# Kernel optimization log

Measured on AMD Instinct MI355X. Metric: run time of the kernel, lower is better.

Reference implementation:

```python
import jax, jax.numpy as jnp
import numpy as np

S_GRID = 7
B_BOX = 2
N_CLS = 20
N_CH = B_BOX * 5 + N_CLS  # 30
LAMBDA_OBJ = 5.0
LAMBDA_NOOBJ = 0.5
CI = np.array([4, 9])
BI = np.array([0, 1, 2, 3, 5, 6, 7, 8])


def setup_inputs() -> dict:
    key = jax.random.key(0)
    k1, k2 = jax.random.split(key)
    batch = 512
    P = jax.random.uniform(k1, (batch, S_GRID, S_GRID, N_CH), dtype=jnp.float32)
    T = jax.random.uniform(k2, (batch, S_GRID, S_GRID, N_CH), dtype=jnp.float32)
    # deterministic object mask: 1/8 of cells are 'object' cells (channel 4 == 1 exactly)
    cell_idx = jnp.arange(batch * S_GRID * S_GRID).reshape(batch, S_GRID, S_GRID)
    obj_mask = (cell_idx % 8 == 0).astype(jnp.float32)
    T = T.at[..., 4].set(obj_mask)
    return {"P": P, "T": T}


def _norm2dnorm(b, S):
    # (cx, cy, w, h) -> (x1, y1, x2, y2) with cx,cy divided by S
    xy = b[:, :2] / S
    wh = b[:, 2:]
    return jnp.concatenate([xy - 0.5 * wh, xy + 0.5 * wh], axis=-1)


def _iou_mat(b1, b2):
    # b1: (N,4), b2: (M,4) -> (N,M) IoU
    lt = jnp.maximum(b1[:, None, :2], b2[None, :, :2])
    rb = jnp.minimum(b1[:, None, 2:], b2[None, :, 2:])
    wh = jnp.clip(rb - lt, 0.0)
    inter = wh[..., 0] * wh[..., 1]
    a1 = (b1[:, 2] - b1[:, 0]) * (b1[:, 3] - b1[:, 1])
    a2 = (b2[:, 2] - b2[:, 0]) * (b2[:, 3] - b2[:, 1])
    return inter / (a1[:, None] + a2[None, :] - inter)


def reference(P, T):
    batch = P.shape[0]
    Pf = P.reshape(-1, N_CH)
    Tf = T.reshape(-1, N_CH)
    # masks computed on concrete data (static counts by construction)
    obj = np.asarray(Tf[:, 4] == 1.0)
    coord_idx = jnp.asarray(np.nonzero(obj)[0])
    noobj_idx = jnp.asarray(np.nonzero(~obj)[0])

    coordP = Pf[coord_idx]
    coordT = Tf[coord_idx]
    noobjP = Pf[noobj_idx]
    noobjT = Tf[noobj_idx]

    ClassP = coordP[:, B_BOX * 5:]
    ClassT = coordT[:, B_BOX * 5:]
    NoObjP = noobjP[:, CI].reshape(-1)
    NoObjT = noobjT[:, CI].reshape(-1)
    ConfP = coordP[:, CI].reshape(-1)          # (2*Ncoord,)
    BBoxP = coordP[:, BI].reshape(-1, 4)       # (2*Ncoord, 4)
    BBoxT = coordT[:, BI].reshape(-1, 4)

    # original torch code does this under no_grad -> stop_gradient
    BP = jax.lax.stop_gradient(_norm2dnorm(BBoxP, float(S_GRID)))
    BT = jax.lax.stop_gradient(_norm2dnorm(BBoxT, float(S_GRID)))
    M = _iou_mat(BP, BT)                       # (NSize, NSize)
    iou = jax.lax.stop_gradient(jnp.max(M, axis=0))
    idx = jnp.argmax(M, axis=0)                # best pred row per target column

    BPg = BP[idx]
    BTg = BT[idx]
    ConfPg = ConfP[idx]

    lossXY = jnp.sum((BPg[:, :2] - BTg[:, :2]) ** 2)
    lossWH = jnp.sum((jnp.sqrt(BPg[:, 2:]) - jnp.sqrt(BTg[:, 2:])) ** 2)
    lossObj = jnp.sum((ConfPg - iou) ** 2)
    lossNObj = jnp.sum((NoObjP - NoObjT) ** 2)
    lossClass = jnp.sum((ClassP - ClassT) ** 2)

    return (LAMBDA_OBJ * (lossXY + lossWH) + LAMBDA_NOOBJ * lossNObj + (lossObj + lossClass)) / batch
```

## Files before the change

kernel.cpp:

```cpp
#include <hip/hip_runtime.h>
#include <stdint.h>

#define S_GRID 7
#define N_CH 30
#define MAXB 8192
#define NTILE 32
#define NCHUNK 80

typedef float float8 __attribute__((ext_vector_type(8)));


__global__ void k_init(float* __restrict__ acc, int* __restrict__ ctr, int* __restrict__ finalCtr) {
    if (threadIdx.x < 4)  acc[threadIdx.x] = 0.0f;
    if (threadIdx.x == 4) *ctr = 0;
    if (threadIdx.x == 5) *finalCtr = 0;
}

__global__ void k_prep(const float* __restrict__ P, const float* __restrict__ T, int ncell,
                       int* __restrict__ ctr,
                       float8* __restrict__ PB8, float4* __restrict__ BT4,
                       float* __restrict__ acc,
                       unsigned long long* __restrict__ maxkey) {
    int gid = blockIdx.x * 256 + threadIdx.x;
    if (gid < MAXB) maxkey[gid] = 0ull;

    int cell = gid;
    float2 pr[15], tr[15];
    if (cell < ncell) {
        const float2* p2 = (const float2*)(P + (size_t)cell * N_CH);
        const float2* t2 = (const float2*)(T + (size_t)cell * N_CH);
        #pragma unroll
        for (int k = 0; k < 15; ++k) { pr[k] = p2[k]; tr[k] = t2[k]; }
    } else {
        #pragma unroll
        for (int k = 0; k < 15; ++k) { pr[k] = make_float2(0.f, 0.f); tr[k] = make_float2(0.f, 0.f); }
    }
    bool obj = (cell < ncell) && (tr[2].x == 1.0f);

    int lane = threadIdx.x & 63;
    unsigned long long bm = __ballot(obj);
    int wcnt = __popcll(bm);
    int base = 0;
    if (lane == 0 && wcnt) base = atomicAdd(ctr, wcnt);
    base = __shfl(base, 0);

    float cls = 0.f, nob = 0.f;
    if (cell < ncell) {
        if (obj) {
            #pragma unroll
            for (int k = 5; k < 15; ++k) {
                float d0 = pr[k].x - tr[k].x, d1 = pr[k].y - tr[k].y;
                cls += d0 * d0 + d1 * d1;
            }
        } else {
            float d0 = pr[2].x - tr[2].x;
            float d1 = pr[4].y - tr[4].y;
            nob = d0 * d0 + d1 * d1;
        }
    }
    #pragma unroll
    for (int o = 32; o; o >>= 1) { cls += __shfl_down(cls, o); nob += __shfl_down(nob, o); }
    if (lane == 0) {
        if (cls != 0.f) atomicAdd(&acc[3], cls);
        if (nob != 0.f) atomicAdd(&acc[2], nob);
    }

    if (obj) {
        int rank = base + __popcll(bm & ((1ull << lane) - 1ull));
        float bx[2][5] = {
            { pr[0].x, pr[0].y, pr[1].x, pr[1].y, pr[2].x },
            { pr[2].y, pr[3].x, pr[3].y, pr[4].x, pr[4].y }
        };
        float tx[2][4] = {
            { tr[0].x, tr[0].y, tr[1].x, tr[1].y },
            { tr[2].y, tr[3].x, tr[3].y, tr[4].x }
        };
        #pragma unroll
        for (int bb = 0; bb < 2; ++bb) {
            int m = 2 * rank + bb;
            if (m < MAXB) {
                float cx = bx[bb][0] / (float)S_GRID, cy = bx[bb][1] / (float)S_GRID;
                float w = bx[bb][2], h = bx[bb][3];
                float8 v;
                v[0] = cx - 0.5f * w; v[1] = cy - 0.5f * h;
                v[2] = cx + 0.5f * w; v[3] = cy + 0.5f * h;
                v[4] = (v[2] - v[0]) * (v[3] - v[1]);
                v[5] = bx[bb][4];
                v[6] = 0.f; v[7] = 0.f;
                PB8[m] = v;
                cx = tx[bb][0] / (float)S_GRID; cy = tx[bb][1] / (float)S_GRID;
                w = tx[bb][2]; h = tx[bb][3];
                BT4[m] = make_float4(cx - 0.5f * w, cy - 0.5f * h, cx + 0.5f * w, cy + 0.5f * h);
            }
        }
    }
}

__global__ void k_match(const float8* __restrict__ PB8, const float4* __restrict__ BT4,
                        const int* __restrict__ ctr,
                        unsigned long long* __restrict__ maxkey) {
    int nb = 2 * (*ctr); if (nb > MAXB) nb = MAXB;
    int tid = threadIdx.x;
    int j = blockIdx.x * 256 + tid;
    if (blockIdx.x * 256 >= nb) return;
    int c = blockIdx.y;
    int chunkLen = (((nb + NCHUNK - 1) / NCHUNK) + 3) & ~3;
    int i0 = c * chunkLen;
    int i1 = min(nb, i0 + chunkLen);
    if (i0 >= i1) return;

    float4 tb = BT4[min(j, nb - 1)];
    float ta = (tb.z - tb.x) * (tb.w - tb.y);
    float bI = -1.f, bS = 1.f;
    int bidx = 0;

    float8 n0 = PB8[i0], n1 = PB8[i0 + 1], n2 = PB8[i0 + 2], n3 = PB8[i0 + 3];
    for (int ib = i0; ib < i1; ib += 4) {
        float8 c0 = n0, c1 = n1, c2 = n2, c3 = n3;
        int nx = ib + 4;
        if (nx < i1) { n0 = PB8[nx]; n1 = PB8[nx + 1]; n2 = PB8[nx + 2]; n3 = PB8[nx + 3]; }
        #define STEP(cc, kk)  {                                                     \
            float lx = fmaxf(tb.x, cc[0]), ly = fmaxf(tb.y, cc[1]);                 \
            float rx = fminf(tb.z, cc[2]), ry = fminf(tb.w, cc[3]);                 \
            float wx = fmaxf(rx - lx, 0.f), wy = fmaxf(ry - ly, 0.f);               \
            float inter = wx * wy;                                                  \
            float sum = ta + cc[4];                                                 \
            bool win = (inter * bS > bI * sum) && ((ib + kk) < i1);                 \
            bI   = win ? inter      : bI;                                           \
            bS   = win ? sum        : bS;                                           \
            bidx = win ? (ib + kk)  : bidx;                                         \
        }
        STEP(c0, 0) STEP(c1, 1) STEP(c2, 2) STEP(c3, 3)
        #undef STEP
    }

    if (j < nb && bI >= 0.f) {
        float iou = bI / (bS - bI);
        unsigned long long key =
            ((unsigned long long)__float_as_uint(iou) << 32) |
            (unsigned long long)(0xFFFFFFFFu - (unsigned)bidx);
        atomicMax(&maxkey[j], key);
    }
}

__global__ void k_final(const float8* __restrict__ PB8, const float4* __restrict__ BT4,
                        const int* __restrict__ ctr,
                        const unsigned long long* __restrict__ maxkey,
                        float* __restrict__ acc, int* __restrict__ finalCtr,
                        float* __restrict__ out, float inv_batch) {
    int nb = 2 * (*ctr); if (nb > MAXB) nb = MAXB;
    int tid = threadIdx.x;
    int j = blockIdx.x * 256 + tid;
    float sxywh = 0.f, sobj = 0.f;
    if (j < nb) {
        unsigned long long key = maxkey[j];
        float iou = __uint_as_float((unsigned)(key >> 32));
        unsigned idx = 0xFFFFFFFFu - (unsigned)(key & 0xFFFFFFFFull);
        float8 pb = PB8[idx];
        float4 bt = BT4[idx];
        float dx = pb[0] - bt.x, dy = pb[1] - bt.y;
        float dw = sqrtf(pb[2]) - sqrtf(bt.z);
        float dh = sqrtf(pb[3]) - sqrtf(bt.w);
        sxywh = dx * dx + dy * dy + dw * dw + dh * dh;
        float dob = pb[5] - iou;
        sobj = dob * dob;
    }
    #pragma unroll
    for (int o = 32; o; o >>= 1) { sxywh += __shfl_down(sxywh, o); sobj += __shfl_down(sobj, o); }
    if ((tid & 63) == 0) {
        if (sxywh != 0.f) atomicAdd(&acc[0], sxywh);
        if (sobj != 0.f)  atomicAdd(&acc[1], sobj);
    }
    __syncthreads();
    if (tid == 0) {
        int old = __hip_atomic_fetch_add(finalCtr, 1, __ATOMIC_ACQ_REL, __HIP_MEMORY_SCOPE_AGENT);
        if (old == NTILE - 1) {
            float a0 = __hip_atomic_load(&acc[0], __ATOMIC_RELAXED, __HIP_MEMORY_SCOPE_AGENT);
            float a1 = __hip_atomic_load(&acc[1], __ATOMIC_RELAXED, __HIP_MEMORY_SCOPE_AGENT);
            float a2 = __hip_atomic_load(&acc[2], __ATOMIC_RELAXED, __HIP_MEMORY_SCOPE_AGENT);
            float a3 = __hip_atomic_load(&acc[3], __ATOMIC_RELAXED, __HIP_MEMORY_SCOPE_AGENT);
            out[0] = (5.0f * a0 + 0.5f * a2 + a1 + a3) * inv_batch;
        }
    }
}

extern "C" void kernel_launch(void* const* d_in, const int* in_sizes, int n_in,
                              void* d_out, int out_size, void* d_ws, size_t ws_size,
                              hipStream_t stream) {
    const float* P = (const float*)d_in[0];
    const float* T = (const float*)d_in[1];
    int ncell = in_sizes[0] / N_CH;
    int batch = ncell / (S_GRID * S_GRID);

    char* ws = (char*)d_ws;
    float* acc      = (float*)ws;
    int*   ctr      = (int*)(ws + 16);
    int*   finalCtr = (int*)(ws + 20);
    unsigned long long* maxkey = (unsigned long long*)(ws + 1024);
    float8* PB8 = (float8*)(ws + 66560);
    float4* BT4 = (float4*)(ws + 328704);

    int nblk = (ncell + 255) / 256;
    k_init <<<1, 64, 0, stream>>>(acc, ctr, finalCtr);
    k_prep <<<nblk, 256, 0, stream>>>(P, T, ncell, ctr, PB8, BT4, acc, maxkey);
    dim3 g3(NTILE, NCHUNK);
    k_match<<<g3, 256, 0, stream>>>(PB8, BT4, ctr, maxkey);
    k_final<<<NTILE, 256, 0, stream>>>(PB8, BT4, ctr, maxkey, acc, finalCtr,
                                       (float*)d_out, 1.0f / (float)batch);
}
```

Baseline: 59.17 us.

## Stage predicted boxes in LDS as float4 and recompute area in match kernel

Predicted boxes are now stored as a compact float4 array, with confidence moved to a separate ConfP array, instead of a padded float8 that carried a precomputed area. Each k_match block copies its chunk of prediction boxes into shared memory once, and every thread then reads from LDS rather than issuing its own global or L1 loads. The box area is recomputed per pair, which adds a few FLOPs in the inner loop, and a __syncthreads is added per block. The goal is to halve the bytes per box and cut redundant global-load traffic in the O(N^2) IoU matching loop.

```diff
diff --git a/kernel.cpp b/kernel.cpp
--- a/kernel.cpp
+++ b/kernel.cpp
@@ -6,8 +6,7 @@
 #define MAXB 8192
 #define NTILE 32
 #define NCHUNK 80
-
-typedef float float8 __attribute__((ext_vector_type(8)));
+#define CHUNK_MAX 104
 
 
 __global__ void k_init(float* __restrict__ acc, int* __restrict__ ctr, int* __restrict__ finalCtr) {
@@ -18,7 +17,8 @@
 
 __global__ void k_prep(const float* __restrict__ P, const float* __restrict__ T, int ncell,
                        int* __restrict__ ctr,
-                       float8* __restrict__ PB8, float4* __restrict__ BT4,
+                       float4* __restrict__ PB4, float4* __restrict__ BT4,
+                       float* __restrict__ ConfP,
                        float* __restrict__ acc,
                        unsigned long long* __restrict__ maxkey) {
     int gid = blockIdx.x * 256 + threadIdx.x;
@@ -81,13 +81,8 @@
             if (m < MAXB) {
                 float cx = bx[bb][0] / (float)S_GRID, cy = bx[bb][1] / (float)S_GRID;
                 float w = bx[bb][2], h = bx[bb][3];
-                float8 v;
-                v[0] = cx - 0.5f * w; v[1] = cy - 0.5f * h;
-                v[2] = cx + 0.5f * w; v[3] = cy + 0.5f * h;
-                v[4] = (v[2] - v[0]) * (v[3] - v[1]);
-                v[5] = bx[bb][4];
-                v[6] = 0.f; v[7] = 0.f;
-                PB8[m] = v;
+                PB4[m] = make_float4(cx - 0.5f * w, cy - 0.5f * h, cx + 0.5f * w, cy + 0.5f * h);
+                ConfP[m] = bx[bb][4];
                 cx = tx[bb][0] / (float)S_GRID; cy = tx[bb][1] / (float)S_GRID;
                 w = tx[bb][2]; h = tx[bb][3];
                 BT4[m] = make_float4(cx - 0.5f * w, cy - 0.5f * h, cx + 0.5f * w, cy + 0.5f * h);
@@ -96,9 +91,10 @@
     }
 }
 
-__global__ void k_match(const float8* __restrict__ PB8, const float4* __restrict__ BT4,
+__global__ void k_match(const float4* __restrict__ PB4, const float4* __restrict__ BT4,
                         const int* __restrict__ ctr,
                         unsigned long long* __restrict__ maxkey) {
+    __shared__ float4 sh[CHUNK_MAX];
     int nb = 2 * (*ctr); if (nb > MAXB) nb = MAXB;
     int tid = threadIdx.x;
     int j = blockIdx.x * 256 + tid;
@@ -109,28 +105,32 @@
     int i1 = min(nb, i0 + chunkLen);
     if (i0 >= i1) return;
 
+    int len = i1 - i0;
+    int padded = (len + 3) & ~3;
+    for (int k = tid; k < padded; k += 256)
+        sh[k] = (k < len) ? PB4[i0 + k] : make_float4(0.f, 0.f, 0.f, 0.f);
+    __syncthreads();
+
     float4 tb = BT4[min(j, nb - 1)];
     float ta = (tb.z - tb.x) * (tb.w - tb.y);
     float bI = -1.f, bS = 1.f;
     int bidx = 0;
 
-    float8 n0 = PB8[i0], n1 = PB8[i0 + 1], n2 = PB8[i0 + 2], n3 = PB8[i0 + 3];
-    for (int ib = i0; ib < i1; ib += 4) {
-        float8 c0 = n0, c1 = n1, c2 = n2, c3 = n3;
-        int nx = ib + 4;
-        if (nx < i1) { n0 = PB8[nx]; n1 = PB8[nx + 1]; n2 = PB8[nx + 2]; n3 = PB8[nx + 3]; }
-        #define STEP(cc, kk)  {                                                     \
-            float lx = fmaxf(tb.x, cc[0]), ly = fmaxf(tb.y, cc[1]);                 \
-            float rx = fminf(tb.z, cc[2]), ry = fminf(tb.w, cc[3]);                 \
+    for (int kb = 0; kb < padded; kb += 4) {
+        float4 b0 = sh[kb], b1 = sh[kb + 1], b2 = sh[kb + 2], b3 = sh[kb + 3];
+        #define STEP(bb, kk)  {                                                     \
+            float lx = fmaxf(tb.x, bb.x), ly = fmaxf(tb.y, bb.y);                   \
+            float rx = fminf(tb.z, bb.z), ry = fminf(tb.w, bb.w);                   \
             float wx = fmaxf(rx - lx, 0.f), wy = fmaxf(ry - ly, 0.f);               \
             float inter = wx * wy;                                                  \
-            float sum = ta + cc[4];                                                 \
-            bool win = (inter * bS > bI * sum) && ((ib + kk) < i1);                 \
-            bI   = win ? inter      : bI;                                           \
-            bS   = win ? sum        : bS;                                           \
-            bidx = win ? (ib + kk)  : bidx;                                         \
-        }
-        STEP(c0, 0) STEP(c1, 1) STEP(c2, 2) STEP(c3, 3)
+            float area = (bb.z - bb.x) * (bb.w - bb.y);                             \
+            float sum = ta + area;                                                  \
+            bool win = (inter * bS > bI * sum) && ((kb + kk) < len);                \
+            bI   = win ? inter          : bI;                                       \
+            bS   = win ? sum            : bS;                                       \
+            bidx = win ? (i0 + kb + kk) : bidx;                                     \
+        }
+        STEP(b0, 0) STEP(b1, 1) STEP(b2, 2) STEP(b3, 3)
         #undef STEP
     }
 
@@ -143,7 +143,8 @@
     }
 }
 
-__global__ void k_final(const float8* __restrict__ PB8, const float4* __restrict__ BT4,
+__global__ void k_final(const float4* __restrict__ PB4, const float4* __restrict__ BT4,
+                        const float* __restrict__ ConfP,
                         const int* __restrict__ ctr,
                         const unsigned long long* __restrict__ maxkey,
                         float* __restrict__ acc, int* __restrict__ finalCtr,
@@ -156,13 +157,14 @@
         unsigned long long key = maxkey[j];
         float iou = __uint_as_float((unsigned)(key >> 32));
         unsigned idx = 0xFFFFFFFFu - (unsigned)(key & 0xFFFFFFFFull);
-        float8 pb = PB8[idx];
+        float4 bp = PB4[idx];
         float4 bt = BT4[idx];
-        float dx = pb[0] - bt.x, dy = pb[1] - bt.y;
-        float dw = sqrtf(pb[2]) - sqrtf(bt.z);
-        float dh = sqrtf(pb[3]) - sqrtf(bt.w);
+        float cp = ConfP[idx];
+        float dx = bp.x - bt.x, dy = bp.y - bt.y;
+        float dw = sqrtf(bp.z) - sqrtf(bt.z);
+        float dh = sqrtf(bp.w) - sqrtf(bt.w);
         sxywh = dx * dx + dy * dy + dw * dw + dh * dh;
-        float dob = pb[5] - iou;
+        float dob = cp - iou;
         sobj = dob * dob;
     }
     #pragma unroll
@@ -197,14 +199,15 @@
     int*   ctr      = (int*)(ws + 16);
     int*   finalCtr = (int*)(ws + 20);
     unsigned long long* maxkey = (unsigned long long*)(ws + 1024);
-    float8* PB8 = (float8*)(ws + 66560);
-    float4* BT4 = (float4*)(ws + 328704);
+    float4* PB4  = (float4*)(ws + 66560);
+    float4* BT4  = (float4*)(ws + 197632);
+    float*  ConfP = (float*)(ws + 328704);
 
     int nblk = (ncell + 255) / 256;
     k_init <<<1, 64, 0, stream>>>(acc, ctr, finalCtr);
-    k_prep <<<nblk, 256, 0, stream>>>(P, T, ncell, ctr, PB8, BT4, acc, maxkey);
+    k_prep <<<nblk, 256, 0, stream>>>(P, T, ncell, ctr, PB4, BT4, ConfP, acc, maxkey);
     dim3 g3(NTILE, NCHUNK);
-    k_match<<<g3, 256, 0, stream>>>(PB8, BT4, ctr, maxkey);
-    k_final<<<NTILE, 256, 0, stream>>>(PB8, BT4, ctr, maxkey, acc, finalCtr,
+    k_match<<<g3, 256, 0, stream>>>(PB4, BT4, ctr, maxkey);
+    k_final<<<NTILE, 256, 0, stream>>>(PB4, BT4, ConfP, ctr, maxkey, acc, finalCtr,
                                        (float*)d_out, 1.0f / (float)batch);
 }
```

New measurement: 57.49 us. 1.03x faster.
